# Performance work log

Measured on AMD Instinct MI355X. Metric: run time of the kernel, lower is better.

Reference implementation:

```python
import jax, jax.numpy as jnp
import numpy as np

B, S, H, N_IN, N_PROC, R = 4, 1024, 1024, 64, 16, 128

def setup_inputs() -> dict:
    key = jax.random.key(0)
    k0, k1, k2, k3, k4 = jax.random.split(key, 5)
    intermediate = jax.random.normal(k0, (B, S, H), dtype=jnp.float32)
    enriched_activations = jax.random.normal(k1, (B, S, N_IN), dtype=jnp.float32)
    # Conv2d(1 -> N_proc, kernel=(5, N_in)), default PyTorch init scale ~ 1/sqrt(fan_in)
    fan_in = 1 * 5 * N_IN
    conv_w = jax.random.uniform(k2, (N_PROC, 1, 5, N_IN), dtype=jnp.float32,
                                minval=-1.0, maxval=1.0) / np.sqrt(fan_in).astype(np.float32)
    conv_b = jnp.zeros((N_PROC,), dtype=jnp.float32)
    down_proj = 0.02 * jax.random.normal(k3, (N_PROC, H, R), dtype=jnp.float32)
    up_proj = 0.02 * jax.random.normal(k4, (N_PROC, R, H), dtype=jnp.float32)
    return {"intermediate": intermediate, "enriched_activations": enriched_activations,
            "conv_w": conv_w, "conv_b": conv_b, "down_proj": down_proj, "up_proj": up_proj}

def reference(intermediate, enriched_activations, conv_w, conv_b, down_proj, up_proj):
    # act_map: [B, 1, S, N_in]; conv kernel (5, N_in) with padding (2, 0) -> [B, N_proc, S, 1]
    act_map = enriched_activations[:, None, :, :]
    pr = jax.lax.conv_general_dilated(
        act_map, conv_w, window_strides=(1, 1), padding=((2, 2), (0, 0)),
        dimension_numbers=("NCHW", "OIHW", "NCHW"))
    pr = pr + conv_b[None, :, None, None]
    # squeeze width, transpose to [B, S, N_proc], sigmoid gate
    process_activations = jax.nn.sigmoid(jnp.transpose(pr[..., 0], (0, 2, 1)))
    # per-expert low-rank transform
    down = jnp.einsum("bsh,nhr->bsnr", intermediate, down_proj)          # [B,S,N,R]
    transformed = jnp.einsum("bsnr,nrh->bsnh", down, up_proj)            # [B,S,N,H]
    # gate-weighted sum over experts (fuses multiply + sum over n)
    output = jnp.einsum("bsnh,bsn->bsh", transformed, process_activations)
    return (output, process_activations)
```

## Files before the change

### kernel.cpp

```cpp
#include <hip/hip_runtime.h>
#include <hip/hip_fp16.h>

#define T_TOK 4096
#define H_DIM 1024
#define NIN   64
#define NP    16
#define R_DIM 128
#define S_DIM 1024
#define N1    (NP * R_DIM)

typedef _Float16 half8  __attribute__((ext_vector_type(8)));
typedef _Float16 half4v __attribute__((ext_vector_type(4)));
typedef float    floatx16 __attribute__((ext_vector_type(16)));

typedef __attribute__((address_space(3))) unsigned char lds_u8_t;
typedef __attribute__((address_space(1))) unsigned char gbl_u8_t;

__device__ __forceinline__ void g2l16(const void* g, void* l) {
  __builtin_amdgcn_global_load_lds((const gbl_u8_t*)g, (lds_u8_t*)l, 16, 0, 0);
}

template <int GATE, int K, int N>
__global__ __launch_bounds__(256)
void gemm_kernel(const _Float16* __restrict__ A, const _Float16* __restrict__ BT,
                 const float* __restrict__ gv, void* __restrict__ Cv) {
  constexpr int NK = K / 64;
  constexpr int GX = N / 128;
  __shared__ __align__(16) _Float16 smem[4][64 * 128];

  const int tid = threadIdx.x, wave = tid >> 6, lane = tid & 63;
  const int id = blockIdx.x;
  const int xcd = id & 7, s = id >> 3;
  const int byi = s / GX + 4 * xcd;
  const int bxi = s % GX;
  const int m0 = byi * 128, n0 = bxi * 128;
  const int wr = (wave >> 1) * 64, wc = (wave & 1) * 64;
  const int rl = lane >> 4, ql = lane & 15;
  const int r = lane & 31, kh = lane >> 5;

  auto stage = [&](const _Float16* __restrict__ base, int off0, int k0,
                   _Float16* dst) {
    #pragma unroll
    for (int c = 0; c < 4; ++c) {
      const int cc = wave * 4 + c;
      const int lrow = cc * 4 + rl;
      const int cl = ql ^ (lrow & 15);
      const int row = lrow + ((cl >> 3) << 6);
      g2l16(base + (size_t)(off0 + row) * K + k0 + (cl & 7) * 8, dst + cc * 512);
    }
  };

  floatx16 acc[2][2];
  #pragma unroll
  for (int i = 0; i < 2; ++i)
    #pragma unroll
    for (int j = 0; j < 2; ++j) acc[i][j] = (floatx16)0.f;

  _Float16 *cA = smem[0], *nA = smem[1], *cB = smem[2], *nB = smem[3];
  stage(A, m0, 0, cA);
  stage(BT, n0, 0, cB);

  #pragma unroll 2
  for (int k = 0; k < NK; ++k) {
    if (k + 1 < NK) {
      stage(A, m0, (k + 1) * 64, nA);
      stage(BT, n0, (k + 1) * 64, nB);
      __builtin_amdgcn_s_waitcnt(0xF78);
    } else {
      __builtin_amdgcn_s_waitcnt(0xF70);
    }
    __builtin_amdgcn_s_barrier();
    __builtin_amdgcn_sched_barrier(0);
    #pragma unroll
    for (int h = 0; h < 4; ++h) {
      const int pA = (2 * h + kh + ((wave >> 1) << 3)) ^ (r & 15);
      const int pB = (2 * h + kh + ((wave & 1) << 3)) ^ (r & 15);
      half8 af[2], bf[2];
      #pragma unroll
      for (int i = 0; i < 2; ++i)
        af[i] = *reinterpret_cast<const half8*>(&cA[(i * 32 + r) * 128 + pA * 8]);
      #pragma unroll
      for (int j = 0; j < 2; ++j)
        bf[j] = *reinterpret_cast<const half8*>(&cB[(j * 32 + r) * 128 + pB * 8]);
      #pragma unroll
      for (int i = 0; i < 2; ++i)
        #pragma unroll
        for (int j = 0; j < 2; ++j)
          acc[i][j] = __builtin_amdgcn_mfma_f32_32x32x16_f16(af[i], bf[j], acc[i][j], 0, 0, 0);
    }
    __builtin_amdgcn_sched_barrier(0);
    __builtin_amdgcn_s_barrier();
    _Float16* t;
    t = cA; cA = nA; nA = t;
    t = cB; cB = nB; nB = t;
  }

  if (GATE) {
    _Float16* C = (_Float16*)Cv;
    #pragma unroll
    for (int i = 0; i < 2; ++i)
      #pragma unroll
      for (int g4 = 0; g4 < 4; ++g4)
        #pragma unroll
        for (int rr = 0; rr < 4; ++rr) {
          const int rowL = wr + i * 32 + rr + 8 * g4 + 4 * kh;
          const float g = gv[(size_t)(m0 + rowL) * NP + bxi];
          #pragma unroll
          for (int j = 0; j < 2; ++j)
            C[(size_t)(m0 + rowL) * N + n0 + wc + j * 32 + r] =
                (_Float16)(acc[i][j][g4 * 4 + rr] * g);
        }
  } else {
    float* C = (float*)Cv;
    #pragma unroll
    for (int i = 0; i < 2; ++i)
      #pragma unroll
      for (int g4 = 0; g4 < 4; ++g4)
        #pragma unroll
        for (int rr = 0; rr < 4; ++rr) {
          const int rowL = wr + i * 32 + rr + 8 * g4 + 4 * kh;
          #pragma unroll
          for (int j = 0; j < 2; ++j)
            C[(size_t)(m0 + rowL) * N + n0 + wc + j * 32 + r] = acc[i][j][g4 * 4 + rr];
        }
  }
}

__global__ __launch_bounds__(256)
void prep_kernel(const float* __restrict__ enr, const float* __restrict__ cw,
                 const float* __restrict__ cb, const float* __restrict__ inter,
                 const float* __restrict__ dproj, const float* __restrict__ uproj,
                 float* __restrict__ gates, _Float16* __restrict__ Xh,
                 _Float16* __restrict__ BT1, _Float16* __restrict__ UT) {
  __shared__ __align__(16) char smem[25664];
  const int tid = threadIdx.x;
  const int bx = blockIdx.x, nb = gridDim.x;
  {
    const float4* src = (const float4*)inter;
    half4v* dst = (half4v*)Xh;
    for (int i = bx * 256 + tid; i < T_TOK * H_DIM / 4; i += nb * 256) {
      float4 v = src[i];
      half4v o;
      o[0] = (_Float16)v.x; o[1] = (_Float16)v.y; o[2] = (_Float16)v.z; o[3] = (_Float16)v.w;
      dst[i] = o;
    }
  }
  if (bx < 256) {
    float (*sw)[321] = (float (*)[321])smem;
    float (*se)[NIN] = (float (*)[NIN])(smem + 20544);
    const int t0 = bx * 16;
    const int b = t0 >> 10, s0 = t0 & 1023;
    for (int i = tid; i < NP * 320; i += 256) sw[i / 320][i % 320] = cw[i];
    for (int i = tid; i < 20 * NIN; i += 256) {
      int rr = i >> 6, c = i & 63, s = s0 + rr - 2;
      se[rr][c] = (s >= 0 && s < S_DIM) ? enr[((size_t)b * S_DIM + s) * NIN + c] : 0.f;
    }
    __syncthreads();
    const int lt = tid >> 4, n = tid & 15;
    float acc = cb[n];
    #pragma unroll
    for (int dh = 0; dh < 5; ++dh) {
      const float* wrow = &sw[n][dh * 64];
      const float* erow = se[lt + dh];
      #pragma unroll
      for (int j = 0; j < NIN; ++j) acc += erow[j] * wrow[j];
    }
    gates[(size_t)(t0 + lt) * NP + n] = 1.f / (1.f + expf(-acc));
    __syncthreads();
  }
  for (int u = bx; u < 4096; u += nb) {
    const float* src; _Float16* dst; int rows, cols, bxt, byt;
    if (u < 2048) {
      int n = u >> 7, rem = u & 127;
      src = dproj + (size_t)n * H_DIM * R_DIM;
      dst = BT1 + (size_t)n * R_DIM * H_DIM;
      rows = H_DIM; cols = R_DIM; bxt = rem & 3; byt = rem >> 2;
    } else {
      int u2 = u - 2048;
      src = uproj; dst = UT; rows = N1; cols = H_DIM;
      bxt = u2 & 31; byt = u2 >> 5;
    }
    float (*tile)[33] = (float (*)[33])smem;
    const int c0 = bxt * 32, r0 = byt * 32;
    const int tx = tid & 31, ty = tid >> 5;
    #pragma unroll
    for (int k = 0; k < 32; k += 8)
      tile[ty + k][tx] = src[(size_t)(r0 + ty + k) * cols + c0 + tx];
    __syncthreads();
    #pragma unroll
    for (int k = 0; k < 32; k += 8)
      dst[(size_t)(c0 + ty + k) * rows + r0 + tx] = (_Float16)tile[tx][ty + k];
    __syncthreads();
  }
}

extern "C" void kernel_launch(void* const* d_in, const int* in_sizes, int n_in,
                              void* d_out, int out_size, void* d_ws, size_t ws_size,
                              hipStream_t stream) {
  const float* inter = (const float*)d_in[0];
  const float* enr   = (const float*)d_in[1];
  const float* convw = (const float*)d_in[2];
  const float* convb = (const float*)d_in[3];
  const float* dproj = (const float*)d_in[4];
  const float* uproj = (const float*)d_in[5];
  float* out   = (float*)d_out;
  float* gates = out + (size_t)T_TOK * H_DIM;

  _Float16* Xh  = (_Float16*)d_ws;
  _Float16* BT1 = Xh  + (size_t)T_TOK * H_DIM;
  _Float16* UT  = BT1 + (size_t)N1 * H_DIM;
  _Float16* Dsc = UT  + (size_t)H_DIM * N1;

  prep_kernel<<<8448, 256, 0, stream>>>(enr, convw, convb, inter, dproj, uproj,
                                        gates, Xh, BT1, UT);
  gemm_kernel<1, H_DIM, N1>
      <<<(N1 / 128) * (T_TOK / 128), 256, 0, stream>>>(Xh, BT1, gates, (void*)Dsc);
  gemm_kernel<0, N1, H_DIM>
      <<<(H_DIM / 128) * (T_TOK / 128), 256, 0, stream>>>(Dsc, UT, nullptr, (void*)out);
}
```

Measured before the change: 133.1 us.

## Split second GEMM along K with atomic accumulation into zeroed output

New measurement: 153.7 us. +15.5%, slower.

```diff
diff --git a/kernel.cpp b/kernel.cpp
--- a/kernel.cpp
+++ b/kernel.cpp
@@ -20,23 +20,29 @@
   __builtin_amdgcn_global_load_lds((const gbl_u8_t*)g, (lds_u8_t*)l, 16, 0, 0);
 }
 
-template <int GATE, int K, int N>
+template <int GATE, int LDK, int KLEN, int N, int SPLITK>
 __global__ __launch_bounds__(256)
 void gemm_kernel(const _Float16* __restrict__ A, const _Float16* __restrict__ BT,
                  const float* __restrict__ gv, void* __restrict__ Cv) {
-  constexpr int NK = K / 64;
+  constexpr int NK = KLEN / 64;
   constexpr int GX = N / 128;
   __shared__ __align__(16) _Float16 smem[4][64 * 128];
 
   const int tid = threadIdx.x, wave = tid >> 6, lane = tid & 63;
   const int id = blockIdx.x;
   const int xcd = id & 7, s = id >> 3;
-  const int byi = s / GX + 4 * xcd;
-  const int bxi = s % GX;
+  constexpr int GRP = GX * SPLITK;
+  const int byi = s / GRP + 4 * xcd;
+  const int rem = s % GRP;
+  const int bxi = rem / SPLITK;
+  const int ks  = rem % SPLITK;
   const int m0 = byi * 128, n0 = bxi * 128;
   const int wr = (wave >> 1) * 64, wc = (wave & 1) * 64;
   const int rl = lane >> 4, ql = lane & 15;
   const int r = lane & 31, kh = lane >> 5;
+
+  const _Float16* Ab = A + (size_t)ks * KLEN;
+  const _Float16* Bb = BT + (size_t)ks * KLEN;
 
   auto stage = [&](const _Float16* __restrict__ base, int off0, int k0,
                    _Float16* dst) {
@@ -46,7 +52,7 @@
       const int lrow = cc * 4 + rl;
       const int cl = ql ^ (lrow & 15);
       const int row = lrow + ((cl >> 3) << 6);
-      g2l16(base + (size_t)(off0 + row) * K + k0 + (cl & 7) * 8, dst + cc * 512);
+      g2l16(base + (size_t)(off0 + row) * LDK + k0 + (cl & 7) * 8, dst + cc * 512);
     }
   };
 
@@ -57,14 +63,14 @@
     for (int j = 0; j < 2; ++j) acc[i][j] = (floatx16)0.f;
 
   _Float16 *cA = smem[0], *nA = smem[1], *cB = smem[2], *nB = smem[3];
-  stage(A, m0, 0, cA);
-  stage(BT, n0, 0, cB);
+  stage(Ab, m0, 0, cA);
+  stage(Bb, n0, 0, cB);
 
   #pragma unroll 2
   for (int k = 0; k < NK; ++k) {
     if (k + 1 < NK) {
-      stage(A, m0, (k + 1) * 64, nA);
-      stage(BT, n0, (k + 1) * 64, nB);
+      stage(Ab, m0, (k + 1) * 64, nA);
+      stage(Bb, n0, (k + 1) * 64, nB);
       __builtin_amdgcn_s_waitcnt(0xF78);
     } else {
       __builtin_amdgcn_s_waitcnt(0xF70);
@@ -110,7 +116,7 @@
             C[(size_t)(m0 + rowL) * N + n0 + wc + j * 32 + r] =
                 (_Float16)(acc[i][j][g4 * 4 + rr] * g);
         }
-  } else {
+  } else if (SPLITK == 1) {
     float* C = (float*)Cv;
     #pragma unroll
     for (int i = 0; i < 2; ++i)
@@ -123,6 +129,20 @@
           for (int j = 0; j < 2; ++j)
             C[(size_t)(m0 + rowL) * N + n0 + wc + j * 32 + r] = acc[i][j][g4 * 4 + rr];
         }
+  } else {
+    float* C = (float*)Cv;
+    #pragma unroll
+    for (int i = 0; i < 2; ++i)
+      #pragma unroll
+      for (int g4 = 0; g4 < 4; ++g4)
+        #pragma unroll
+        for (int rr = 0; rr < 4; ++rr) {
+          const int rowL = wr + i * 32 + rr + 8 * g4 + 4 * kh;
+          #pragma unroll
+          for (int j = 0; j < 2; ++j)
+            unsafeAtomicAdd(&C[(size_t)(m0 + rowL) * N + n0 + wc + j * 32 + r],
+                            acc[i][j][g4 * 4 + rr]);
+        }
   }
 }
 
@@ -131,7 +151,8 @@
                  const float* __restrict__ cb, const float* __restrict__ inter,
                  const float* __restrict__ dproj, const float* __restrict__ uproj,
                  float* __restrict__ gates, _Float16* __restrict__ Xh,
-                 _Float16* __restrict__ BT1, _Float16* __restrict__ UT) {
+                 _Float16* __restrict__ BT1, _Float16* __restrict__ UT,
+                 float* __restrict__ outz) {
   __shared__ __align__(16) char smem[25664];
   const int tid = threadIdx.x;
   const int bx = blockIdx.x, nb = gridDim.x;
@@ -145,6 +166,13 @@
       dst[i] = o;
     }
   }
+  if (bx >= 4096) {
+    const int i = (bx - 4096) * 256 + tid;
+    if (i < T_TOK * H_DIM / 4) {
+      float4 z; z.x = 0.f; z.y = 0.f; z.z = 0.f; z.w = 0.f;
+      ((float4*)outz)[i] = z;
+    }
+  }
   if (bx < 256) {
     float (*sw)[321] = (float (*)[321])smem;
     float (*se)[NIN] = (float (*)[NIN])(smem + 20544);
@@ -212,9 +240,9 @@
   _Float16* Dsc = UT  + (size_t)H_DIM * N1;
 
   prep_kernel<<<8448, 256, 0, stream>>>(enr, convw, convb, inter, dproj, uproj,
-                                        gates, Xh, BT1, UT);
-  gemm_kernel<1, H_DIM, N1>
+                                        gates, Xh, BT1, UT, out);
+  gemm_kernel<1, H_DIM, H_DIM, N1, 1>
       <<<(N1 / 128) * (T_TOK / 128), 256, 0, stream>>>(Xh, BT1, gates, (void*)Dsc);
-  gemm_kernel<0, N1, H_DIM>
-      <<<(H_DIM / 128) * (T_TOK / 128), 256, 0, stream>>>(Dsc, UT, nullptr, (void*)out);
-}
+  gemm_kernel<0, N1, N1 / 2, H_DIM, 2>
+      <<<(H_DIM / 128) * (T_TOK / 128) * 2, 256, 0, stream>>>(Dsc, UT, nullptr, (void*)out);
+}
```

## Enlarge GEMM block tile to 256x128 with eight waves and dynamic LDS

Applied to the files above, without the earlier changes.

Result: slower. 143.1 us (+7.5%).

```diff
diff --git a/kernel.cpp b/kernel.cpp
--- a/kernel.cpp
+++ b/kernel.cpp
@@ -21,32 +21,42 @@
 }
 
 template <int GATE, int K, int N>
-__global__ __launch_bounds__(256)
-void gemm_kernel(const _Float16* __restrict__ A, const _Float16* __restrict__ BT,
-                 const float* __restrict__ gv, void* __restrict__ Cv) {
+__global__ __launch_bounds__(512)
+void gemm8p(const _Float16* __restrict__ A, const _Float16* __restrict__ BT,
+            const float* __restrict__ gv, void* __restrict__ Cv) {
   constexpr int NK = K / 64;
   constexpr int GX = N / 128;
-  __shared__ __align__(16) _Float16 smem[4][64 * 128];
+  extern __shared__ __align__(16) _Float16 dlds[];
 
   const int tid = threadIdx.x, wave = tid >> 6, lane = tid & 63;
   const int id = blockIdx.x;
   const int xcd = id & 7, s = id >> 3;
-  const int byi = s / GX + 4 * xcd;
+  const int byi = s / GX + 2 * xcd;
   const int bxi = s % GX;
-  const int m0 = byi * 128, n0 = bxi * 128;
-  const int wr = (wave >> 1) * 64, wc = (wave & 1) * 64;
+  const int m0 = byi * 256, n0 = bxi * 128;
+  const int wmr = wave >> 1, wnc = wave & 1;
+  const int wr = wmr * 64, wc = wnc * 64;
   const int rl = lane >> 4, ql = lane & 15;
   const int r = lane & 31, kh = lane >> 5;
 
-  auto stage = [&](const _Float16* __restrict__ base, int off0, int k0,
-                   _Float16* dst) {
+  auto stageA = [&](const _Float16* __restrict__ base, int k0, _Float16* dst) {
     #pragma unroll
     for (int c = 0; c < 4; ++c) {
       const int cc = wave * 4 + c;
       const int lrow = cc * 4 + rl;
       const int cl = ql ^ (lrow & 15);
+      const int row = lrow + ((cl >> 3) << 7);
+      g2l16(base + (size_t)(m0 + row) * K + k0 + (cl & 7) * 8, dst + cc * 512);
+    }
+  };
+  auto stageB = [&](const _Float16* __restrict__ base, int k0, _Float16* dst) {
+    #pragma unroll
+    for (int c = 0; c < 2; ++c) {
+      const int cc = wave * 2 + c;
+      const int lrow = cc * 4 + rl;
+      const int cl = ql ^ (lrow & 15);
       const int row = lrow + ((cl >> 3) << 6);
-      g2l16(base + (size_t)(off0 + row) * K + k0 + (cl & 7) * 8, dst + cc * 512);
+      g2l16(base + (size_t)(n0 + row) * K + k0 + (cl & 7) * 8, dst + cc * 512);
     }
   };
 
@@ -56,16 +66,17 @@
     #pragma unroll
     for (int j = 0; j < 2; ++j) acc[i][j] = (floatx16)0.f;
 
-  _Float16 *cA = smem[0], *nA = smem[1], *cB = smem[2], *nB = smem[3];
-  stage(A, m0, 0, cA);
-  stage(BT, n0, 0, cB);
+  _Float16 *cA = dlds,          *nA = dlds + 16384;
+  _Float16 *cB = dlds + 32768,  *nB = dlds + 40960;
+  stageA(A, 0, cA);
+  stageB(BT, 0, cB);
 
   #pragma unroll 2
   for (int k = 0; k < NK; ++k) {
     if (k + 1 < NK) {
-      stage(A, m0, (k + 1) * 64, nA);
-      stage(BT, n0, (k + 1) * 64, nB);
-      __builtin_amdgcn_s_waitcnt(0xF78);
+      stageA(A, (k + 1) * 64, nA);
+      stageB(BT, (k + 1) * 64, nB);
+      __builtin_amdgcn_s_waitcnt(0xF76);
     } else {
       __builtin_amdgcn_s_waitcnt(0xF70);
     }
@@ -73,12 +84,13 @@
     __builtin_amdgcn_sched_barrier(0);
     #pragma unroll
     for (int h = 0; h < 4; ++h) {
-      const int pA = (2 * h + kh + ((wave >> 1) << 3)) ^ (r & 15);
-      const int pB = (2 * h + kh + ((wave & 1) << 3)) ^ (r & 15);
+      const int pA = (2 * h + kh + ((wmr >> 1) << 3)) ^ (r & 15);
+      const int pB = (2 * h + kh + (wnc << 3)) ^ (r & 15);
       half8 af[2], bf[2];
       #pragma unroll
       for (int i = 0; i < 2; ++i)
-        af[i] = *reinterpret_cast<const half8*>(&cA[(i * 32 + r) * 128 + pA * 8]);
+        af[i] = *reinterpret_cast<const half8*>(
+            &cA[((wmr & 1) * 64 + i * 32 + r) * 128 + pA * 8]);
       #pragma unroll
       for (int j = 0; j < 2; ++j)
         bf[j] = *reinterpret_cast<const half8*>(&cB[(j * 32 + r) * 128 + pB * 8]);
@@ -211,10 +223,15 @@
   _Float16* UT  = BT1 + (size_t)N1 * H_DIM;
   _Float16* Dsc = UT  + (size_t)H_DIM * N1;
 
+  hipFuncSetAttribute((const void*)gemm8p<1, H_DIM, N1>,
+                      hipFuncAttributeMaxDynamicSharedMemorySize, 98304);
+  hipFuncSetAttribute((const void*)gemm8p<0, N1, H_DIM>,
+                      hipFuncAttributeMaxDynamicSharedMemorySize, 98304);
+
   prep_kernel<<<8448, 256, 0, stream>>>(enr, convw, convb, inter, dproj, uproj,
                                         gates, Xh, BT1, UT);
-  gemm_kernel<1, H_DIM, N1>
-      <<<(N1 / 128) * (T_TOK / 128), 256, 0, stream>>>(Xh, BT1, gates, (void*)Dsc);
-  gemm_kernel<0, N1, H_DIM>
-      <<<(H_DIM / 128) * (T_TOK / 128), 256, 0, stream>>>(Dsc, UT, nullptr, (void*)out);
-}
+  gemm8p<1, H_DIM, N1>
+      <<<(T_TOK / 256) * (N1 / 128), 512, 98304, stream>>>(Xh, BT1, gates, (void*)Dsc);
+  gemm8p<0, N1, H_DIM>
+      <<<(T_TOK / 256) * (H_DIM / 128), 512, 98304, stream>>>(Dsc, UT, nullptr, (void*)out);
+}
```

## Use 256x256-tile 8-wave GEMM with interleaved staging for down-projection

Applied to the files above, without the earlier changes.

Measured after the change: 148.3 us. 11.5% more time.

```diff
diff --git a/kernel.cpp b/kernel.cpp
--- a/kernel.cpp
+++ b/kernel.cpp
@@ -18,6 +18,106 @@
 
 __device__ __forceinline__ void g2l16(const void* g, void* l) {
   __builtin_amdgcn_global_load_lds((const gbl_u8_t*)g, (lds_u8_t*)l, 16, 0, 0);
+}
+
+template <int K, int N>
+__global__ __launch_bounds__(512, 2)
+void gemm256(const _Float16* __restrict__ A, const _Float16* __restrict__ BT,
+             const float* __restrict__ gv, _Float16* __restrict__ C) {
+  constexpr int NK = K / 64;
+  extern __shared__ __align__(16) _Float16 dlds[];
+
+  const int tid = threadIdx.x, wave = tid >> 6, lane = tid & 63;
+  const int id = blockIdx.x;
+  const int xcd = id & 7, s = id >> 3;
+  const int byi = (s >> 3) + 2 * xcd;
+  const int bxi = s & 7;
+  const int m0 = byi * 256, n0 = bxi * 256;
+  const int wmr = wave >> 2;
+  const int wnc = wave & 3;
+  const int nb3 = wnc & 1;
+  const int rl = lane >> 4, ql = lane & 15;
+  const int r = lane & 31, kh = lane >> 5;
+
+  auto stageAq = [&](int q, int k0, _Float16* dst) {
+    const int cc = q * 8 + wave;
+    const int pr = cc * 4 + rl;
+    const int hf = pr >> 6, lrow = pr & 63;
+    const int cl = ql ^ (lrow & 15);
+    const int mrow = hf * 128 + lrow + ((cl >> 3) << 6);
+    g2l16(A + (size_t)(m0 + mrow) * K + k0 + (cl & 7) * 8, dst + cc * 512);
+  };
+  auto stageBq = [&](int q, int k0, _Float16* dst) {
+    const int cc = q * 8 + wave;
+    const int pr = cc * 4 + rl;
+    const int hf = pr >> 6, lrow = pr & 63;
+    const int cl = ql ^ (lrow & 15);
+    const int nrow = hf * 128 + lrow + ((cl >> 3) << 6);
+    g2l16(BT + (size_t)(n0 + nrow) * K + k0 + (cl & 7) * 8, dst + cc * 512);
+  };
+
+  floatx16 acc[4][2];
+  #pragma unroll
+  for (int g = 0; g < 4; ++g)
+    #pragma unroll
+    for (int j = 0; j < 2; ++j) acc[g][j] = (floatx16)0.f;
+
+  #pragma unroll
+  for (int q = 0; q < 4; ++q) { stageAq(q, 0, dlds); stageBq(q, 0, dlds + 16384); }
+  __builtin_amdgcn_s_waitcnt(0xF70);
+  __builtin_amdgcn_s_barrier();
+
+  for (int kt = 0; kt < NK; ++kt) {
+    _Float16* cA = dlds + (kt & 1) * 32768;
+    _Float16* cB = cA + 16384;
+    _Float16* nA = dlds + ((kt + 1) & 1) * 32768;
+    _Float16* nB = nA + 16384;
+    const _Float16* Ah = cA + wmr * 8192;
+    const _Float16* Bh = cB + (wnc >> 1) * 8192;
+    #pragma unroll
+    for (int q = 0; q < 4; ++q) {
+      const int p = q & 1;
+      const int j = q >> 1;
+      half8 af[2][4], bf[4];
+      #pragma unroll
+      for (int h = 0; h < 4; ++h) {
+        const int pA = (2 * h + kh + (p << 3)) ^ (r & 15);
+        af[0][h] = *reinterpret_cast<const half8*>(&Ah[(r) * 128 + pA * 8]);
+        af[1][h] = *reinterpret_cast<const half8*>(&Ah[(32 + r) * 128 + pA * 8]);
+        const int pB = (2 * h + kh + (nb3 << 3)) ^ (r & 15);
+        bf[h] = *reinterpret_cast<const half8*>(&Bh[(j * 32 + r) * 128 + pB * 8]);
+      }
+      if (kt + 1 < NK) { stageAq(q, (kt + 1) * 64, nA); stageBq(q, (kt + 1) * 64, nB); }
+      __builtin_amdgcn_s_barrier();
+      __builtin_amdgcn_s_setprio(1);
+      #pragma unroll
+      for (int h = 0; h < 4; ++h) {
+        acc[p * 2 + 0][j] = __builtin_amdgcn_mfma_f32_32x32x16_f16(af[0][h], bf[h], acc[p * 2 + 0][j], 0, 0, 0);
+        acc[p * 2 + 1][j] = __builtin_amdgcn_mfma_f32_32x32x16_f16(af[1][h], bf[h], acc[p * 2 + 1][j], 0, 0, 0);
+      }
+      __builtin_amdgcn_s_setprio(0);
+      if (q == 3 && kt + 1 < NK)
+        __builtin_amdgcn_s_waitcnt(0xF70);
+      __builtin_amdgcn_s_barrier();
+    }
+  }
+
+  const int neuron = bxi * 2 + (wnc >> 1);
+  #pragma unroll
+  for (int g = 0; g < 4; ++g) {
+    const int rbase = wmr * 128 + (g >> 1) * 64 + (g & 1) * 32;
+    #pragma unroll
+    for (int g4 = 0; g4 < 4; ++g4)
+      #pragma unroll
+      for (int rr = 0; rr < 4; ++rr) {
+        const int rowL = rbase + rr + 8 * g4 + 4 * kh;
+        const float gt = gv[(size_t)(m0 + rowL) * NP + neuron];
+        #pragma unroll
+        for (int j = 0; j < 2; ++j)
+          C[(size_t)(m0 + rowL) * N + n0 + wnc * 64 + j * 32 + r] =
+              (_Float16)(acc[g][j][g4 * 4 + rr] * gt);
+      }
+  }
 }
 
 template <int GATE, int K, int N>
@@ -211,10 +311,13 @@
   _Float16* UT  = BT1 + (size_t)N1 * H_DIM;
   _Float16* Dsc = UT  + (size_t)H_DIM * N1;
 
+  hipFuncSetAttribute((const void*)gemm256<H_DIM, N1>,
+                      hipFuncAttributeMaxDynamicSharedMemorySize, 131072);
+
   prep_kernel<<<8448, 256, 0, stream>>>(enr, convw, convb, inter, dproj, uproj,
                                         gates, Xh, BT1, UT);
-  gemm_kernel<1, H_DIM, N1>
-      <<<(N1 / 128) * (T_TOK / 128), 256, 0, stream>>>(Xh, BT1, gates, (void*)Dsc);
+  gemm256<H_DIM, N1>
+      <<<(T_TOK / 256) * (N1 / 256), 512, 131072, stream>>>(Xh, BT1, gates, Dsc);
   gemm_kernel<0, N1, H_DIM>
       <<<(H_DIM / 128) * (T_TOK / 128), 256, 0, stream>>>(Dsc, UT, nullptr, (void*)out);
 }
```
